# Performance work log

Measured on AMD Instinct MI355X. Metric: run time of the kernel, lower is better.

Reference implementation:

```python
import jax, jax.numpy as jnp
import numpy as np

HEAD_SIZE = 64
NEG_INF = float('-inf')


def setup_inputs() -> dict:
    key = jax.random.key(0)
    ks = jax.random.split(key, 4)
    B, S, H, D = 8, 4096, 1024, HEAD_SIZE
    scale = 1.0 / np.sqrt(H)
    return {
        'x': jax.random.normal(ks[0], (B, S, H), dtype=jnp.float32),
        'Wq': jax.random.normal(ks[1], (H, D), dtype=jnp.float32) * scale,
        'bq': jnp.zeros((D,), dtype=jnp.float32),
        'Wk': jax.random.normal(ks[2], (H, D), dtype=jnp.float32) * scale,
        'bk': jnp.zeros((D,), dtype=jnp.float32),
        'Wv': jax.random.normal(ks[3], (H, D), dtype=jnp.float32) * scale,
        'bv': jnp.zeros((D,), dtype=jnp.float32),
    }


def reference(x, Wq, bq, Wk, bk, Wv, bv):
    # x: [B, S, H]; projections -> [B, S, D]
    B, S, H = x.shape
    q = jnp.einsum('bsh,hd->bsd', x, Wq) + bq
    k = jnp.einsum('bsh,hd->bsd', x, Wk) + bk
    v = jnp.einsum('bsh,hd->bsd', x, Wv) + bv
    # raw scores [B, S, S]
    scores = jnp.einsum('bqd,bkd->bqk', q, k)
    # causal mask applied BEFORE scaling (matches original; -inf/scale == -inf)
    causal = jnp.tril(jnp.ones((S, S), dtype=bool))
    scores = jnp.where(causal, scores, NEG_INF)
    scale = 1.0 / jnp.sqrt(jnp.asarray(q.shape[-1], dtype=scores.dtype))
    attn = jax.nn.softmax(scores * scale, axis=-1)
    # dropout = 0.0 (eval) -> identity
    return jnp.einsum('bqk,bkd->bqd', attn, v)
```

## Files before the change

### kernel.cpp

```cpp
#include <hip/hip_runtime.h>
#include <hip/hip_bf16.h>
#include <math.h>

#define SEQ 4096
#define HID 1024
#define DH  64
#define NB  8
#define QSCALE 0.18033688011112042f

typedef unsigned short ushort_t;
typedef unsigned int   uint_t;
typedef __attribute__((ext_vector_type(8))) short  bf16x8;
typedef __attribute__((ext_vector_type(4))) float  f32x4;
typedef __attribute__((ext_vector_type(4))) uint_t u32x4;

static __device__ __forceinline__ ushort_t f2bf(float f) {
    __hip_bfloat16 h = __float2bfloat16(f);
    return *reinterpret_cast<ushort_t*>(&h);
}
static __device__ __forceinline__ ushort_t f2bf_fast(float f) {
    uint_t u = __float_as_uint(f);
    return (ushort_t)((u + 0x8000u) >> 16);
}

__global__ __launch_bounds__(256) void prep_w(
    const float* __restrict__ Wq, const float* __restrict__ Wk,
    const float* __restrict__ Wv, ushort_t* __restrict__ wts)
{
    __shared__ ushort_t tr[64][72];
    const int bx   = blockIdx.x;
    const int mmat = bx >> 4;
    const int kt   = bx & 15;
    const float* W  = (mmat == 0) ? Wq : (mmat == 1) ? Wk : Wv;
    const float  sc = (mmat == 0) ? QSCALE : 1.0f;

    const int t  = threadIdx.x;
    const int kr = t >> 2, kc = (t & 3) * 16;
    const float* src = W + (size_t)(kt * 64 + kr) * DH + kc;
    float4 a0 = *(const float4*)(src);
    float4 a1 = *(const float4*)(src + 4);
    float4 a2 = *(const float4*)(src + 8);
    float4 a3 = *(const float4*)(src + 12);
    float vv[16] = {a0.x,a0.y,a0.z,a0.w, a1.x,a1.y,a1.z,a1.w,
                    a2.x,a2.y,a2.z,a2.w, a3.x,a3.y,a3.z,a3.w};
    #pragma unroll
    for (int i = 0; i < 16; ++i) tr[kr][kc + i] = f2bf(vv[i] * sc);
    __syncthreads();

    const int cl = t >> 2, jc = (t & 3) * 16;
    const int c  = mmat * 64 + cl;
    ushort_t* dst = wts + kt * 12288 + c * 64;
    #pragma unroll
    for (int jj = 0; jj < 16; ++jj) {
        int j = jc + jj;
        dst[((j >> 3) ^ (cl & 7)) * 8 + (j & 7)] = tr[j][cl];
    }
}

__global__ __launch_bounds__(256) void qkv_proj(
    const float* __restrict__ x, const ushort_t* __restrict__ wts,
    const float* __restrict__ bq, const float* __restrict__ bk,
    const float* __restrict__ bv,
    ushort_t* __restrict__ qimg, ushort_t* __restrict__ kimg,
    ushort_t* __restrict__ vimg)
{
    __shared__ ushort_t xs[2][64][72];
    __shared__ ushort_t bw[2][12288];

    const int t  = threadIdx.x;
    const int w  = t >> 6, l = t & 63, lr = l & 15, lg = l >> 4;
    const int row0 = blockIdx.x * 64;
    const int sxr = t >> 2, sxc = (t & 3) * 16;
    const int ch0 = (lg ^ (lr & 7)) * 8;
    const int ch1 = ((lg + 4) ^ (lr & 7)) * 8;

    f32x4 acc[4][3];
    #pragma unroll
    for (int i = 0; i < 4; ++i)
        #pragma unroll
        for (int j = 0; j < 3; ++j) acc[i][j] = (f32x4){0.f,0.f,0.f,0.f};

    float4 Xf[4];
    u32x4  Bf[6];
    {
        const float* xr = x + (size_t)(row0 + sxr) * HID + sxc;
        Xf[0] = *(const float4*)(xr);      Xf[1] = *(const float4*)(xr + 4);
        Xf[2] = *(const float4*)(xr + 8);  Xf[3] = *(const float4*)(xr + 12);
        const char* bsrc = (const char*)wts + t * 16;
        #pragma unroll
        for (int i = 0; i < 6; ++i) Bf[i] = *(const u32x4*)(bsrc + i * 4096);
    }

    for (int kt = 0; kt < 16; ++kt) {
        const int buf = kt & 1;
        {
            u32x4 p0, p1;
            p0.x = (uint_t)f2bf(Xf[0].x) | ((uint_t)f2bf(Xf[0].y) << 16);
            p0.y = (uint_t)f2bf(Xf[0].z) | ((uint_t)f2bf(Xf[0].w) << 16);
            p0.z = (uint_t)f2bf(Xf[1].x) | ((uint_t)f2bf(Xf[1].y) << 16);
            p0.w = (uint_t)f2bf(Xf[1].z) | ((uint_t)f2bf(Xf[1].w) << 16);
            p1.x = (uint_t)f2bf(Xf[2].x) | ((uint_t)f2bf(Xf[2].y) << 16);
            p1.y = (uint_t)f2bf(Xf[2].z) | ((uint_t)f2bf(Xf[2].w) << 16);
            p1.z = (uint_t)f2bf(Xf[3].x) | ((uint_t)f2bf(Xf[3].y) << 16);
            p1.w = (uint_t)f2bf(Xf[3].z) | ((uint_t)f2bf(Xf[3].w) << 16);
            *(u32x4*)&xs[buf][sxr][sxc]     = p0;
            *(u32x4*)&xs[buf][sxr][sxc + 8] = p1;
            char* bdst = (char*)&bw[buf][0] + t * 16;
            #pragma unroll
            for (int i = 0; i < 6; ++i) *(u32x4*)(bdst + i * 4096) = Bf[i];
        }
        __syncthreads();
        if (kt < 15) {
            const float* xr = x + (size_t)(row0 + sxr) * HID + (kt + 1) * 64 + sxc;
            Xf[0] = *(const float4*)(xr);      Xf[1] = *(const float4*)(xr + 4);
            Xf[2] = *(const float4*)(xr + 8);  Xf[3] = *(const float4*)(xr + 12);
            const char* bsrc = (const char*)wts + (kt + 1) * 24576 + t * 16;
            #pragma unroll
            for (int i = 0; i < 6; ++i) Bf[i] = *(const u32x4*)(bsrc + i * 4096);
        }
        bf16x8 af0[4], af1[4];
        #pragma unroll
        for (int rt = 0; rt < 4; ++rt) {
            af0[rt] = *(bf16x8*)&xs[buf][rt * 16 + lr][lg * 8];
            af1[rt] = *(bf16x8*)&xs[buf][rt * 16 + lr][lg * 8 + 32];
        }
        #pragma unroll
        for (int ctl = 0; ctl < 3; ++ctl) {
            const int c = (w * 3 + ctl) * 16 + lr;
            bf16x8 b0 = *(bf16x8*)&bw[buf][c * 64 + ch0];
            bf16x8 b1 = *(bf16x8*)&bw[buf][c * 64 + ch1];
            #pragma unroll
            for (int rt = 0; rt < 4; ++rt) {
                acc[rt][ctl] = __builtin_amdgcn_mfma_f32_16x16x32_bf16(
                    af0[rt], b0, acc[rt][ctl], 0, 0, 0);
                acc[rt][ctl] = __builtin_amdgcn_mfma_f32_16x16x32_bf16(
                    af1[rt], b1, acc[rt][ctl], 0, 0, 0);
            }
        }
    }

    #pragma unroll
    for (int ctl = 0; ctl < 3; ++ctl) {
        const int c    = (w * 3 + ctl) * 16 + lr;
        const int mmat = c >> 6;
        const int cc   = c & 63;
        const float* bp = (mmat == 0) ? bq : (mmat == 1) ? bk : bv;
        const float bias = bp[cc] * (mmat == 0 ? QSCALE : 1.0f);
        #pragma unroll
        for (int rt = 0; rt < 4; ++rt)
            #pragma unroll
            for (int r = 0; r < 4; ++r) {
                const int s = row0 + rt * 16 + lg * 4 + r;
                const ushort_t v = f2bf(acc[rt][ctl][r] + bias);
                if (mmat == 0)
                    qimg[(size_t)s * 64 + cc] = v;
                else if (mmat == 1)
                    kimg[(size_t)(s >> 6) * 4096 + (s & 63) * 64 +
                         ((cc >> 3) ^ (s & 7)) * 8 + (cc & 7)] = v;
                else
                    vimg[(size_t)(s >> 6) * 4096 + (size_t)cc * 64 +
                         (((s & 63) >> 3) ^ (cc & 7)) * 8 + (s & 7)] = v;
            }
    }
}

__global__ __launch_bounds__(256) void attn(
    const ushort_t* __restrict__ qimg, const ushort_t* __restrict__ kimg,
    const ushort_t* __restrict__ vimg, float* __restrict__ outg)
{
    __shared__ ushort_t kvs[2][8192];
    __shared__ ushort_t ps[64][76];

    const int t  = threadIdx.x;
    const int w  = t >> 6, l = t & 63, lr = l & 15, lg = l >> 4;
    const int bx = blockIdx.x;
    const int qt = 63 - (bx >> 3);
    const int b  = bx & 7;
    const int q0 = qt * 64;
    const int ch0 = (lg ^ (lr & 7)) * 8;
    const int ch1 = ((lg + 4) ^ (lr & 7)) * 8;

    bf16x8 qf0, qf1;
    {
        const ushort_t* qp = qimg + (size_t)(b * SEQ + q0 + w * 16 + lr) * 64 + lg * 8;
        qf0 = *(const bf16x8*)(qp);
        qf1 = *(const bf16x8*)(qp + 32);
    }
    bf16x8 ones;
    #pragma unroll
    for (int i = 0; i < 8; ++i) ones[i] = (short)0x3F80;

    f32x4 o[4], accl;
    #pragma unroll
    for (int dt = 0; dt < 4; ++dt) o[dt] = (f32x4){0.f,0.f,0.f,0.f};
    accl = (f32x4){0.f,0.f,0.f,0.f};

    const size_t tbase = (size_t)b * 64 * 4096;
    u32x4 pre[4];
    {
        const char* ksrc = (const char*)(kimg + tbase);
        const char* vsrc = (const char*)(vimg + tbase);
        pre[0] = *(const u32x4*)(ksrc + t * 16);
        pre[1] = *(const u32x4*)(ksrc + t * 16 + 4096);
        pre[2] = *(const u32x4*)(vsrc + t * 16);
        pre[3] = *(const u32x4*)(vsrc + t * 16 + 4096);
    }

    for (int kt = 0; kt <= qt; ++kt) {
        const int buf = kt & 1;
        {
            char* dst = (char*)&kvs[buf][0] + t * 16;
            *(u32x4*)(dst)          = pre[0];
            *(u32x4*)(dst + 4096)   = pre[1];
            *(u32x4*)(dst + 8192)   = pre[2];
            *(u32x4*)(dst + 12288)  = pre[3];
        }
        __syncthreads();
        if (kt < qt) {
            const char* ksrc = (const char*)(kimg + tbase) + (kt + 1) * 8192;
            const char* vsrc = (const char*)(vimg + tbase) + (kt + 1) * 8192;
            pre[0] = *(const u32x4*)(ksrc + t * 16);
            pre[1] = *(const u32x4*)(ksrc + t * 16 + 4096);
            pre[2] = *(const u32x4*)(vsrc + t * 16);
            pre[3] = *(const u32x4*)(vsrc + t * 16 + 4096);
        }
        const ushort_t* kb = &kvs[buf][0];
        f32x4 s[4];
        #pragma unroll
        for (int ct = 0; ct < 4; ++ct) s[ct] = (f32x4){0.f,0.f,0.f,0.f};
        #pragma unroll
        for (int ct = 0; ct < 4; ++ct) {
            const int rowb = (ct * 16 + lr) * 64;
            bf16x8 kf0 = *(const bf16x8*)(kb + rowb + ch0);
            bf16x8 kf1 = *(const bf16x8*)(kb + rowb + ch1);
            s[ct] = __builtin_amdgcn_mfma_f32_16x16x32_bf16(qf0, kf0, s[ct], 0, 0, 0);
            s[ct] = __builtin_amdgcn_mfma_f32_16x16x32_bf16(qf1, kf1, s[ct], 0, 0, 0);
        }

        if (kt == qt) {
            #pragma unroll
            for (int r = 0; r < 4; ++r) {
                const int qr = w * 16 + lg * 4 + r;
                #pragma unroll
                for (int ct = 0; ct < 4; ++ct) {
                    float sv = ((ct * 16 + lr) > qr) ? -INFINITY : s[ct][r];
                    float p  = __builtin_amdgcn_exp2f(sv);
                    ps[w * 16 + lg * 4 + r][ct * 16 + lr] = f2bf_fast(p);
                }
            }
        } else {
            #pragma unroll
            for (int r = 0; r < 4; ++r)
                #pragma unroll
                for (int ct = 0; ct < 4; ++ct) {
                    float p = __builtin_amdgcn_exp2f(s[ct][r]);
                    ps[w * 16 + lg * 4 + r][ct * 16 + lr] = f2bf_fast(p);
                }
        }
        asm volatile("s_waitcnt lgkmcnt(0)" ::: "memory");

        bf16x8 pf0 = *(const bf16x8*)&ps[w * 16 + lr][lg * 8];
        bf16x8 pf1 = *(const bf16x8*)&ps[w * 16 + lr][lg * 8 + 32];
        accl = __builtin_amdgcn_mfma_f32_16x16x32_bf16(pf0, ones, accl, 0, 0, 0);
        accl = __builtin_amdgcn_mfma_f32_16x16x32_bf16(pf1, ones, accl, 0, 0, 0);
        const ushort_t* vb = &kvs[buf][4096];
        #pragma unroll
        for (int dt = 0; dt < 4; ++dt) {
            const int rowb = (dt * 16 + lr) * 64;
            bf16x8 vf0 = *(const bf16x8*)(vb + rowb + ch0);
            bf16x8 vf1 = *(const bf16x8*)(vb + rowb + ch1);
            o[dt] = __builtin_amdgcn_mfma_f32_16x16x32_bf16(pf0, vf0, o[dt], 0, 0, 0);
            o[dt] = __builtin_amdgcn_mfma_f32_16x16x32_bf16(pf1, vf1, o[dt], 0, 0, 0);
        }
    }

    #pragma unroll
    for (int r = 0; r < 4; ++r) {
        const float inv = 1.0f / accl[r];
        float* orow = outg + ((size_t)b * SEQ + q0 + w * 16 + lg * 4 + r) * 64;
        #pragma unroll
        for (int dt = 0; dt < 4; ++dt)
            orow[dt * 16 + lr] = o[dt][r] * inv;
    }
}

extern "C" void kernel_launch(void* const* d_in, const int* in_sizes, int n_in,
                              void* d_out, int out_size, void* d_ws, size_t ws_size,
                              hipStream_t stream) {
    const float* x  = (const float*)d_in[0];
    const float* Wq = (const float*)d_in[1];
    const float* bq = (const float*)d_in[2];
    const float* Wk = (const float*)d_in[3];
    const float* bk = (const float*)d_in[4];
    const float* Wv = (const float*)d_in[5];
    const float* bv = (const float*)d_in[6];
    float* out = (float*)d_out;

    const size_t per = (size_t)NB * SEQ * DH;
    ushort_t* q   = (ushort_t*)d_ws;
    ushort_t* k   = q + per;
    ushort_t* v   = k + per;
    ushort_t* wts = v + per;

    prep_w  <<<dim3(48),  256, 0, stream>>>(Wq, Wk, Wv, wts);
    qkv_proj<<<dim3(512), 256, 0, stream>>>(x, wts, bq, bk, bv, q, k, v);
    attn    <<<dim3(512), 256, 0, stream>>>(q, k, v, out);
}
```

Before: 263.5 us.

## Use direct global-to-LDS loads with triple buffering and software-pipeline softmax

K/V tiles are now fetched with global_load_lds straight into shared memory, into three rotating buffers, instead of being staged through registers. The loop is also software-pipelined: QK^T for the current tile is issued while exp/PV for the previous tile runs, and the masked diagonal tile is handled after the loop. The aim is to cut register pressure and VGPR-to-LDS store traffic, and to overlap MFMA work with the exponentials. In exchange the kernel uses more LDS, and correctness depends on the loads having completed before the barrier, since no explicit vmcnt wait is added.

Measured after the change: 271.6 us. 1.03x slower.

```diff
diff --git a/kernel.cpp b/kernel.cpp
--- a/kernel.cpp
+++ b/kernel.cpp
@@ -21,6 +21,12 @@
 static __device__ __forceinline__ ushort_t f2bf_fast(float f) {
     uint_t u = __float_as_uint(f);
     return (ushort_t)((u + 0x8000u) >> 16);
+}
+
+static __device__ __forceinline__ void gld_lds16(const void* g, void* s) {
+    __builtin_amdgcn_global_load_lds(
+        (const __attribute__((address_space(1))) void*)g,
+        (__attribute__((address_space(3))) void*)s, 16, 0, 0);
 }
 
 __global__ __launch_bounds__(256) void prep_w(
@@ -168,7 +174,7 @@
     const ushort_t* __restrict__ qimg, const ushort_t* __restrict__ kimg,
     const ushort_t* __restrict__ vimg, float* __restrict__ outg)
 {
-    __shared__ ushort_t kvs[2][8192];
+    __shared__ ushort_t kvs[3][8192];
     __shared__ ushort_t ps[64][76];
 
     const int t  = threadIdx.x;
@@ -190,65 +196,50 @@
     #pragma unroll
     for (int i = 0; i < 8; ++i) ones[i] = (short)0x3F80;
 
-    f32x4 o[4], accl;
+    f32x4 o[4], accl, s[4];
     #pragma unroll
     for (int dt = 0; dt < 4; ++dt) o[dt] = (f32x4){0.f,0.f,0.f,0.f};
     accl = (f32x4){0.f,0.f,0.f,0.f};
-
-    const size_t tbase = (size_t)b * 64 * 4096;
-    u32x4 pre[4];
+    #pragma unroll
+    for (int ct = 0; ct < 4; ++ct) s[ct] = (f32x4){0.f,0.f,0.f,0.f};
+
+    const char* kbase = (const char*)kimg + (size_t)b * 524288;
+    const char* vbase = (const char*)vimg + (size_t)b * 524288;
+    const int wo = w * 1024;
+    const int lo = l * 16;
+
     {
-        const char* ksrc = (const char*)(kimg + tbase);
-        const char* vsrc = (const char*)(vimg + tbase);
-        pre[0] = *(const u32x4*)(ksrc + t * 16);
-        pre[1] = *(const u32x4*)(ksrc + t * 16 + 4096);
-        pre[2] = *(const u32x4*)(vsrc + t * 16);
-        pre[3] = *(const u32x4*)(vsrc + t * 16 + 4096);
+        char* lk = (char*)&kvs[0][0];
+        gld_lds16(kbase + wo + lo,        lk + wo);
+        gld_lds16(kbase + wo + lo + 4096, lk + wo + 4096);
+        gld_lds16(vbase + wo + lo,        lk + wo + 8192);
+        gld_lds16(vbase + wo + lo + 4096, lk + wo + 12288);
     }
 
     for (int kt = 0; kt <= qt; ++kt) {
-        const int buf = kt & 1;
-        {
-            char* dst = (char*)&kvs[buf][0] + t * 16;
-            *(u32x4*)(dst)          = pre[0];
-            *(u32x4*)(dst + 4096)   = pre[1];
-            *(u32x4*)(dst + 8192)   = pre[2];
-            *(u32x4*)(dst + 12288)  = pre[3];
-        }
+        const int cur = kt % 3;
         __syncthreads();
         if (kt < qt) {
-            const char* ksrc = (const char*)(kimg + tbase) + (kt + 1) * 8192;
-            const char* vsrc = (const char*)(vimg + tbase) + (kt + 1) * 8192;
-            pre[0] = *(const u32x4*)(ksrc + t * 16);
-            pre[1] = *(const u32x4*)(ksrc + t * 16 + 4096);
-            pre[2] = *(const u32x4*)(vsrc + t * 16);
-            pre[3] = *(const u32x4*)(vsrc + t * 16 + 4096);
-        }
-        const ushort_t* kb = &kvs[buf][0];
-        f32x4 s[4];
-        #pragma unroll
-        for (int ct = 0; ct < 4; ++ct) s[ct] = (f32x4){0.f,0.f,0.f,0.f};
+            const int   nxt = (kt + 1) % 3;
+            const char* ks  = kbase + (size_t)(kt + 1) * 8192;
+            const char* vs  = vbase + (size_t)(kt + 1) * 8192;
+            char*       lk  = (char*)&kvs[nxt][0];
+            gld_lds16(ks + wo + lo,        lk + wo);
+            gld_lds16(ks + wo + lo + 4096, lk + wo + 4096);
+            gld_lds16(vs + wo + lo,        lk + wo + 8192);
+            gld_lds16(vs + wo + lo + 8192 - 4096, lk + wo + 12288);
+        }
+
+        const ushort_t* kb = &kvs[cur][0];
+        bf16x8 kf0[4], kf1[4];
         #pragma unroll
         for (int ct = 0; ct < 4; ++ct) {
             const int rowb = (ct * 16 + lr) * 64;
-            bf16x8 kf0 = *(const bf16x8*)(kb + rowb + ch0);
-            bf16x8 kf1 = *(const bf16x8*)(kb + rowb + ch1);
-            s[ct] = __builtin_amdgcn_mfma_f32_16x16x32_bf16(qf0, kf0, s[ct], 0, 0, 0);
-            s[ct] = __builtin_amdgcn_mfma_f32_16x16x32_bf16(qf1, kf1, s[ct], 0, 0, 0);
-        }
-
-        if (kt == qt) {
-            #pragma unroll
-            for (int r = 0; r < 4; ++r) {
-                const int qr = w * 16 + lg * 4 + r;
-                #pragma unroll
-                for (int ct = 0; ct < 4; ++ct) {
-                    float sv = ((ct * 16 + lr) > qr) ? -INFINITY : s[ct][r];
-                    float p  = __builtin_amdgcn_exp2f(sv);
-                    ps[w * 16 + lg * 4 + r][ct * 16 + lr] = f2bf_fast(p);
-                }
-            }
-        } else {
+            kf0[ct] = *(const bf16x8*)(kb + rowb + ch0);
+            kf1[ct] = *(const bf16x8*)(kb + rowb + ch1);
+        }
+
+        if (kt > 0) {
             #pragma unroll
             for (int r = 0; r < 4; ++r)
                 #pragma unroll
@@ -257,13 +248,50 @@
                     ps[w * 16 + lg * 4 + r][ct * 16 + lr] = f2bf_fast(p);
                 }
         }
-        asm volatile("s_waitcnt lgkmcnt(0)" ::: "memory");
-
+
+        f32x4 sn[4];
+        #pragma unroll
+        for (int ct = 0; ct < 4; ++ct) {
+            sn[ct] = (f32x4){0.f,0.f,0.f,0.f};
+            sn[ct] = __builtin_amdgcn_mfma_f32_16x16x32_bf16(qf0, kf0[ct], sn[ct], 0, 0, 0);
+            sn[ct] = __builtin_amdgcn_mfma_f32_16x16x32_bf16(qf1, kf1[ct], sn[ct], 0, 0, 0);
+        }
+
+        if (kt > 0) {
+            bf16x8 pf0 = *(const bf16x8*)&ps[w * 16 + lr][lg * 8];
+            bf16x8 pf1 = *(const bf16x8*)&ps[w * 16 + lr][lg * 8 + 32];
+            accl = __builtin_amdgcn_mfma_f32_16x16x32_bf16(pf0, ones, accl, 0, 0, 0);
+            accl = __builtin_amdgcn_mfma_f32_16x16x32_bf16(pf1, ones, accl, 0, 0, 0);
+            const ushort_t* vb = &kvs[(kt - 1) % 3][4096];
+            #pragma unroll
+            for (int dt = 0; dt < 4; ++dt) {
+                const int rowb = (dt * 16 + lr) * 64;
+                bf16x8 vf0 = *(const bf16x8*)(vb + rowb + ch0);
+                bf16x8 vf1 = *(const bf16x8*)(vb + rowb + ch1);
+                o[dt] = __builtin_amdgcn_mfma_f32_16x16x32_bf16(pf0, vf0, o[dt], 0, 0, 0);
+                o[dt] = __builtin_amdgcn_mfma_f32_16x16x32_bf16(pf1, vf1, o[dt], 0, 0, 0);
+            }
+        }
+        #pragma unroll
+        for (int ct = 0; ct < 4; ++ct) s[ct] = sn[ct];
+    }
+
+    {
+        #pragma unroll
+        for (int r = 0; r < 4; ++r) {
+            const int qr = w * 16 + lg * 4 + r;
+            #pragma unroll
+            for (int ct = 0; ct < 4; ++ct) {
+                float sv = ((ct * 16 + lr) > qr) ? -INFINITY : s[ct][r];
+                float p  = __builtin_amdgcn_exp2f(sv);
+                ps[w * 16 + lg * 4 + r][ct * 16 + lr] = f2bf_fast(p);
+            }
+        }
         bf16x8 pf0 = *(const bf16x8*)&ps[w * 16 + lr][lg * 8];
         bf16x8 pf1 = *(const bf16x8*)&ps[w * 16 + lr][lg * 8 + 32];
         accl = __builtin_amdgcn_mfma_f32_16x16x32_bf16(pf0, ones, accl, 0, 0, 0);
         accl = __builtin_amdgcn_mfma_f32_16x16x32_bf16(pf1, ones, accl, 0, 0, 0);
-        const ushort_t* vb = &kvs[buf][4096];
+        const ushort_t* vb = &kvs[qt % 3][4096];
         #pragma unroll
         for (int dt = 0; dt < 4; ++dt) {
             const int rowb = (dt * 16 + lr) * 64;
```

## Use direct global-to-LDS loads and transposed MFMA layout in attention kernel

Applied to the files above, without the earlier changes.

Replaces register-staged K/V prefetch with global_load_lds direct copies into the alternate LDS buffer, removing VGPR staging and the LDS store step. Swaps the MFMA operand order so each lane holds four consecutive keys or dims. That allows packed 8-byte P stores, vectorised float4 output stores, and a row sum accumulated in registers plus shuffles instead of an extra ones-MFMA. It also changes the block-to-tile mapping for indices of 256 and above, and uses the faster bf16 rounding in the projection kernel. One risk: the single barrier per iteration must still order the async LDS writes against reads of the previous buffer.

Result: slower. 273.4 us (+3.8%).

```diff
diff --git a/kernel.cpp b/kernel.cpp
--- a/kernel.cpp
+++ b/kernel.cpp
@@ -13,6 +13,7 @@
 typedef __attribute__((ext_vector_type(8))) short  bf16x8;
 typedef __attribute__((ext_vector_type(4))) float  f32x4;
 typedef __attribute__((ext_vector_type(4))) uint_t u32x4;
+typedef __attribute__((ext_vector_type(2))) uint_t u32x2;
 
 static __device__ __forceinline__ ushort_t f2bf(float f) {
     __hip_bfloat16 h = __float2bfloat16(f);
@@ -21,6 +22,15 @@
 static __device__ __forceinline__ ushort_t f2bf_fast(float f) {
     uint_t u = __float_as_uint(f);
     return (ushort_t)((u + 0x8000u) >> 16);
+}
+static __device__ __forceinline__ uint_t bfpair(float lo, float hi) {
+    return (uint_t)f2bf_fast(lo) | ((uint_t)f2bf_fast(hi) << 16);
+}
+
+static __device__ __forceinline__ void gld_lds16(const void* g, void* s) {
+    __builtin_amdgcn_global_load_lds(
+        (const __attribute__((address_space(1))) void*)g,
+        (__attribute__((address_space(3))) void*)s, 16, 0, 0);
 }
 
 __global__ __launch_bounds__(256) void prep_w(
@@ -95,14 +105,14 @@
         const int buf = kt & 1;
         {
             u32x4 p0, p1;
-            p0.x = (uint_t)f2bf(Xf[0].x) | ((uint_t)f2bf(Xf[0].y) << 16);
-            p0.y = (uint_t)f2bf(Xf[0].z) | ((uint_t)f2bf(Xf[0].w) << 16);
-            p0.z = (uint_t)f2bf(Xf[1].x) | ((uint_t)f2bf(Xf[1].y) << 16);
-            p0.w = (uint_t)f2bf(Xf[1].z) | ((uint_t)f2bf(Xf[1].w) << 16);
-            p1.x = (uint_t)f2bf(Xf[2].x) | ((uint_t)f2bf(Xf[2].y) << 16);
-            p1.y = (uint_t)f2bf(Xf[2].z) | ((uint_t)f2bf(Xf[2].w) << 16);
-            p1.z = (uint_t)f2bf(Xf[3].x) | ((uint_t)f2bf(Xf[3].y) << 16);
-            p1.w = (uint_t)f2bf(Xf[3].z) | ((uint_t)f2bf(Xf[3].w) << 16);
+            p0.x = bfpair(Xf[0].x, Xf[0].y);
+            p0.y = bfpair(Xf[0].z, Xf[0].w);
+            p0.z = bfpair(Xf[1].x, Xf[1].y);
+            p0.w = bfpair(Xf[1].z, Xf[1].w);
+            p1.x = bfpair(Xf[2].x, Xf[2].y);
+            p1.y = bfpair(Xf[2].z, Xf[2].w);
+            p1.z = bfpair(Xf[3].x, Xf[3].y);
+            p1.w = bfpair(Xf[3].z, Xf[3].w);
             *(u32x4*)&xs[buf][sxr][sxc]     = p0;
             *(u32x4*)&xs[buf][sxr][sxc + 8] = p1;
             char* bdst = (char*)&bw[buf][0] + t * 16;
@@ -169,118 +179,117 @@
     const ushort_t* __restrict__ vimg, float* __restrict__ outg)
 {
     __shared__ ushort_t kvs[2][8192];
-    __shared__ ushort_t ps[64][76];
+    __shared__ ushort_t ps[64][72];
 
     const int t  = threadIdx.x;
-    const int w  = t >> 6, l = t & 63, lr = l & 15, lg = l >> 4;
+    const int w  = t >> 6, l = t & 63, lr = l & 15, g = l >> 4;
     const int bx = blockIdx.x;
-    const int qt = 63 - (bx >> 3);
+    const int qt = (bx < 256) ? (63 - (bx >> 3)) : ((bx - 256) >> 3);
     const int b  = bx & 7;
     const int q0 = qt * 64;
-    const int ch0 = (lg ^ (lr & 7)) * 8;
-    const int ch1 = ((lg + 4) ^ (lr & 7)) * 8;
+    const int ch0 = (g ^ (lr & 7)) * 8;
+    const int ch1 = ((g + 4) ^ (lr & 7)) * 8;
+    const int qq  = q0 + w * 16 + lr;
 
     bf16x8 qf0, qf1;
     {
-        const ushort_t* qp = qimg + (size_t)(b * SEQ + q0 + w * 16 + lr) * 64 + lg * 8;
+        const ushort_t* qp = qimg + (size_t)(b * SEQ + qq) * 64 + g * 8;
         qf0 = *(const bf16x8*)(qp);
         qf1 = *(const bf16x8*)(qp + 32);
     }
-    bf16x8 ones;
-    #pragma unroll
-    for (int i = 0; i < 8; ++i) ones[i] = (short)0x3F80;
-
-    f32x4 o[4], accl;
+
+    f32x4 o[4];
     #pragma unroll
     for (int dt = 0; dt < 4; ++dt) o[dt] = (f32x4){0.f,0.f,0.f,0.f};
-    accl = (f32x4){0.f,0.f,0.f,0.f};
-
-    const size_t tbase = (size_t)b * 64 * 4096;
-    u32x4 pre[4];
+    float lpart = 0.f;
+
+    const char* kbase = (const char*)kimg + (size_t)b * 524288;
+    const char* vbase = (const char*)vimg + (size_t)b * 524288;
+    const int wo = w * 1024;
+    const int lo = l * 16;
+
     {
-        const char* ksrc = (const char*)(kimg + tbase);
-        const char* vsrc = (const char*)(vimg + tbase);
-        pre[0] = *(const u32x4*)(ksrc + t * 16);
-        pre[1] = *(const u32x4*)(ksrc + t * 16 + 4096);
-        pre[2] = *(const u32x4*)(vsrc + t * 16);
-        pre[3] = *(const u32x4*)(vsrc + t * 16 + 4096);
+        char* lk = (char*)&kvs[0][0];
+        gld_lds16(kbase + wo + lo,        lk + wo);
+        gld_lds16(kbase + wo + lo + 4096, lk + wo + 4096);
+        gld_lds16(vbase + wo + lo,        lk + wo + 8192);
+        gld_lds16(vbase + wo + lo + 4096, lk + wo + 12288);
     }
 
     for (int kt = 0; kt <= qt; ++kt) {
-        const int buf = kt & 1;
-        {
-            char* dst = (char*)&kvs[buf][0] + t * 16;
-            *(u32x4*)(dst)          = pre[0];
-            *(u32x4*)(dst + 4096)   = pre[1];
-            *(u32x4*)(dst + 8192)   = pre[2];
-            *(u32x4*)(dst + 12288)  = pre[3];
-        }
+        const int cur = kt & 1;
         __syncthreads();
         if (kt < qt) {
-            const char* ksrc = (const char*)(kimg + tbase) + (kt + 1) * 8192;
-            const char* vsrc = (const char*)(vimg + tbase) + (kt + 1) * 8192;
-            pre[0] = *(const u32x4*)(ksrc + t * 16);
-            pre[1] = *(const u32x4*)(ksrc + t * 16 + 4096);
-            pre[2] = *(const u32x4*)(vsrc + t * 16);
-            pre[3] = *(const u32x4*)(vsrc + t * 16 + 4096);
-        }
-        const ushort_t* kb = &kvs[buf][0];
+            const char* ks = kbase + (size_t)(kt + 1) * 8192;
+            const char* vs = vbase + (size_t)(kt + 1) * 8192;
+            char*       lk = (char*)&kvs[cur ^ 1][0];
+            gld_lds16(ks + wo + lo,        lk + wo);
+            gld_lds16(ks + wo + lo + 4096, lk + wo + 4096);
+            gld_lds16(vs + wo + lo,        lk + wo + 8192);
+            gld_lds16(vs + wo + lo + 4096, lk + wo + 12288);
+        }
+
+        const ushort_t* kb = &kvs[cur][0];
         f32x4 s[4];
-        #pragma unroll
-        for (int ct = 0; ct < 4; ++ct) s[ct] = (f32x4){0.f,0.f,0.f,0.f};
         #pragma unroll
         for (int ct = 0; ct < 4; ++ct) {
             const int rowb = (ct * 16 + lr) * 64;
             bf16x8 kf0 = *(const bf16x8*)(kb + rowb + ch0);
             bf16x8 kf1 = *(const bf16x8*)(kb + rowb + ch1);
-            s[ct] = __builtin_amdgcn_mfma_f32_16x16x32_bf16(qf0, kf0, s[ct], 0, 0, 0);
-            s[ct] = __builtin_amdgcn_mfma_f32_16x16x32_bf16(qf1, kf1, s[ct], 0, 0, 0);
+            s[ct] = (f32x4){0.f,0.f,0.f,0.f};
+            s[ct] = __builtin_amdgcn_mfma_f32_16x16x32_bf16(kf0, qf0, s[ct], 0, 0, 0);
+            s[ct] = __builtin_amdgcn_mfma_f32_16x16x32_bf16(kf1, qf1, s[ct], 0, 0, 0);
         }
 
         if (kt == qt) {
-            #pragma unroll
-            for (int r = 0; r < 4; ++r) {
-                const int qr = w * 16 + lg * 4 + r;
-                #pragma unroll
-                for (int ct = 0; ct < 4; ++ct) {
-                    float sv = ((ct * 16 + lr) > qr) ? -INFINITY : s[ct][r];
-                    float p  = __builtin_amdgcn_exp2f(sv);
-                    ps[w * 16 + lg * 4 + r][ct * 16 + lr] = f2bf_fast(p);
-                }
+            const int kvb = kt * 64 + g * 4;
+            #pragma unroll
+            for (int ct = 0; ct < 4; ++ct) {
+                float p0 = ((kvb + ct*16 + 0) > qq) ? 0.f : __builtin_amdgcn_exp2f(s[ct][0]);
+                float p1 = ((kvb + ct*16 + 1) > qq) ? 0.f : __builtin_amdgcn_exp2f(s[ct][1]);
+                float p2 = ((kvb + ct*16 + 2) > qq) ? 0.f : __builtin_amdgcn_exp2f(s[ct][2]);
+                float p3 = ((kvb + ct*16 + 3) > qq) ? 0.f : __builtin_amdgcn_exp2f(s[ct][3]);
+                lpart += (p0 + p1) + (p2 + p3);
+                u32x2 pk = { bfpair(p0, p1), bfpair(p2, p3) };
+                *(u32x2*)&ps[w * 16 + lr][ct * 16 + g * 4] = pk;
             }
         } else {
             #pragma unroll
-            for (int r = 0; r < 4; ++r)
-                #pragma unroll
-                for (int ct = 0; ct < 4; ++ct) {
-                    float p = __builtin_amdgcn_exp2f(s[ct][r]);
-                    ps[w * 16 + lg * 4 + r][ct * 16 + lr] = f2bf_fast(p);
-                }
+            for (int ct = 0; ct < 4; ++ct) {
+                float p0 = __builtin_amdgcn_exp2f(s[ct][0]);
+                float p1 = __builtin_amdgcn_exp2f(s[ct][1]);
+                float p2 = __builtin_amdgcn_exp2f(s[ct][2]);
+                float p3 = __builtin_amdgcn_exp2f(s[ct][3]);
+                lpart += (p0 + p1) + (p2 + p3);
+                u32x2 pk = { bfpair(p0, p1), bfpair(p2, p3) };
+                *(u32x2*)&ps[w * 16 + lr][ct * 16 + g * 4] = pk;
+            }
         }
         asm volatile("s_waitcnt lgkmcnt(0)" ::: "memory");
 
-        bf16x8 pf0 = *(const bf16x8*)&ps[w * 16 + lr][lg * 8];
-        bf16x8 pf1 = *(const bf16x8*)&ps[w * 16 + lr][lg * 8 + 32];
-        accl = __builtin_amdgcn_mfma_f32_16x16x32_bf16(pf0, ones, accl, 0, 0, 0);
-        accl = __builtin_amdgcn_mfma_f32_16x16x32_bf16(pf1, ones, accl, 0, 0, 0);
-        const ushort_t* vb = &kvs[buf][4096];
+        bf16x8 pf0 = *(const bf16x8*)&ps[w * 16 + lr][g * 8];
+        bf16x8 pf1 = *(const bf16x8*)&ps[w * 16 + lr][32 + g * 8];
+        const ushort_t* vb = &kvs[cur][4096];
         #pragma unroll
         for (int dt = 0; dt < 4; ++dt) {
             const int rowb = (dt * 16 + lr) * 64;
             bf16x8 vf0 = *(const bf16x8*)(vb + rowb + ch0);
             bf16x8 vf1 = *(const bf16x8*)(vb + rowb + ch1);
-            o[dt] = __builtin_amdgcn_mfma_f32_16x16x32_bf16(pf0, vf0, o[dt], 0, 0, 0);
-            o[dt] = __builtin_amdgcn_mfma_f32_16x16x32_bf16(pf1, vf1, o[dt], 0, 0, 0);
-        }
-    }
-
-    #pragma unroll
-    for (int r = 0; r < 4; ++r) {
-        const float inv = 1.0f / accl[r];
-        float* orow = outg + ((size_t)b * SEQ + q0 + w * 16 + lg * 4 + r) * 64;
-        #pragma unroll
-        for (int dt = 0; dt < 4; ++dt)
-            orow[dt * 16 + lr] = o[dt][r] * inv;
+            o[dt] = __builtin_amdgcn_mfma_f32_16x16x32_bf16(vf0, pf0, o[dt], 0, 0, 0);
+            o[dt] = __builtin_amdgcn_mfma_f32_16x16x32_bf16(vf1, pf1, o[dt], 0, 0, 0);
+        }
+    }
+
+    lpart += __shfl_xor(lpart, 16);
+    lpart += __shfl_xor(lpart, 32);
+    const float inv = 1.0f / lpart;
+
+    float* orow = outg + (size_t)(b * SEQ + qq) * 64;
+    #pragma unroll
+    for (int dt = 0; dt < 4; ++dt) {
+        float4 val = { o[dt][0] * inv, o[dt][1] * inv,
+                       o[dt][2] * inv, o[dt][3] * inv };
+        *(float4*)&orow[dt * 16 + g * 4] = val;
     }
 }
 
```
